# Performance work log

Measured on AMD Instinct MI355X. Metric: run time of the kernel, lower is better.

The kernel has to match this reference:

```python
import jax, jax.numpy as jnp
import numpy as np

# Dims
B, S, D = 4, 4096, 1024
H, NB, A = 4, 4096, 4          # hashes, buckets, associativity
DK, DV, DT = 64, 128, 32        # key dim, value (mem) dim, vsa tag dim
BITS = 12                       # log2(NB)
TEMP = 1.0
VSA_W = 1.0
TANH_SCALE = 1.0
ETA = 0.1
WRITE_THR = 0.5
MATCH_THR = 0.0
NOV_THR = 0.0
EPS = 1e-6


def _l2n(x):
    return x / (jnp.linalg.norm(x, axis=-1, keepdims=True) + EPS)


def setup_inputs() -> dict:
    key = jax.random.key(0)
    ks = jax.random.split(key, 13)
    sc = 0.02
    return {
        "u": jax.random.normal(ks[0], (B, S, D), jnp.float32),
        "memK": jax.random.normal(ks[1], (H, NB, A, DK), jnp.float32),
        "memV": jax.random.normal(ks[2], (H, NB, A, DV), jnp.float32),
        "memT": jnp.tanh(jax.random.normal(ks[3], (H, NB, A, DT), jnp.float32)),
        "Wq": jax.random.normal(ks[4], (DK, D), jnp.float32) * sc,
        "Wwk": jax.random.normal(ks[5], (DK, D), jnp.float32) * sc,
        "Wv": jax.random.normal(ks[6], (DV, D), jnp.float32) * sc,
        "Wo": jax.random.normal(ks[7], (D, DV), jnp.float32) * sc,
        "Wg": jax.random.normal(ks[8], (1, D), jnp.float32) * sc,
        "bg": jnp.zeros((1,), jnp.float32),
        "Wvsa": jax.random.normal(ks[9], (DK, DT), jnp.float32) * sc,
        "R": jax.random.normal(ks[10], (H, DK, BITS), jnp.float32),
    }


def reference(u, memK, memV, memT, Wq, Wwk, Wv, Wo, Wg, bg, Wvsa, R):
    N = B * S
    uf = u.reshape(N, D)

    # ---- routing: sign-bit LSH over query key -> bucket index per hash ----
    qkey = uf @ Wq.T                                     # [N, DK]
    bits = (jnp.einsum("nd,hdk->nhk", qkey, R) > 0).astype(jnp.int32)
    pw = (2 ** jnp.arange(BITS, dtype=jnp.int32))
    idx = (bits * pw).sum(-1)                            # [N, H] bucket ids
    hh = jnp.arange(H)[None, :]                          # [1, H]

    # ---- associative gather read ----
    Kg = memK[hh, idx]                                   # [N, H, A, DK]
    Vg = memV[hh, idx]                                   # [N, H, A, DV]
    Tg = memT[hh, idx]                                   # [N, H, A, DT]
    qtag = jnp.tanh(TANH_SCALE * (qkey @ Wvsa))          # [N, DT]
    sc = (jnp.einsum("nd,nhad->nha", qkey, Kg) / np.sqrt(DK)
          + VSA_W * jnp.einsum("nt,nhat->nha", qtag, Tg) / np.sqrt(DT))
    w = jax.nn.softmax(sc.reshape(N, H * A) / TEMP, axis=-1)
    read = jnp.einsum("nk,nkd->nd", w, Vg.reshape(N, H * A, DV))
    y = (read @ Wo.T).reshape(B, S, D)

    # ---- gated scatter write with EMA + novelty ----
    wkey = uf @ Wwk.T                                    # [N, DK]
    wval = uf @ Wv.T                                     # [N, DV]
    gate = jax.nn.sigmoid(uf @ Wg.T + bg)                # [N, 1]
    wmask = (gate > WRITE_THR).astype(u.dtype)           # [N, 1]
    wtag = jnp.tanh(TANH_SCALE * (wkey @ Wvsa))          # [N, DT]

    sim = jnp.einsum("nd,nhad->nha", _l2n(wkey), _l2n(Kg))   # [N,H,A]
    astar = jnp.argmax(sim, axis=-1)                         # [N,H]
    bsim = jnp.max(sim, axis=-1)                             # [N,H]
    take = lambda G: jnp.take_along_axis(G, astar[:, :, None, None], axis=2)[:, :, 0]
    Kbest, Vbest, Tbest = take(Kg), take(Vg), take(Tg)       # [N,H,·]

    tagsim = jnp.einsum("nt,nhat->nha", _l2n(wtag), _l2n(Tg))
    novelty = 1.0 - jnp.max(tagsim, axis=-1)                 # [N,H]

    eff = (ETA * gate * wmask
           * (bsim >= MATCH_THR).astype(u.dtype)
           * (novelty >= NOV_THR).astype(u.dtype))           # [N,H]

    dK = eff[..., None] * (wkey[:, None, :] - Kbest)
    dV = eff[..., None] * (wval[:, None, :] - Vbest)
    dT = eff[..., None] * (wtag[:, None, :] - Tbest)
    Knew = memK.at[hh, idx, astar].add(dK)
    Vnew = memV.at[hh, idx, astar].add(dV)
    Tnew = memT.at[hh, idx, astar].add(dT)
    return y, Knew, Vnew, Tnew
```

## Files before the change

kernel.cpp:

```cpp
#include <hip/hip_runtime.h>
#include <hip/hip_bf16.h>
#include <math.h>

#define NTOK    16384
#define DMODEL  1024
#define HN      4
#define NBUCKET 4096
#define ASSOC   4
#define DKEY    64
#define DVAL    128
#define DTAG    32
#define NBITS   12
#define EPSV    1e-6f

typedef __bf16 bf16x8 __attribute__((ext_vector_type(8)));
typedef float  f32x4  __attribute__((ext_vector_type(4)));
typedef float  f32x2  __attribute__((ext_vector_type(2)));

__device__ __forceinline__ unsigned short f2bf_raw(float f) {
    __hip_bfloat16 h = __float2bfloat16(f);
    return *(unsigned short*)&h;
}

__global__ __launch_bounds__(256) void gemm_mfma(const float* __restrict__ A,
                                                 const float* __restrict__ B,
                                                 float* __restrict__ C,
                                                 int M, int N, int K) {
    __shared__ __align__(16) unsigned short As[4][128][8];
    __shared__ __align__(16) unsigned short Bs[4][128][8];
    const int t    = threadIdx.x;
    const int lane = t & 63;
    const int w    = t >> 6;
    const int wm   = (w & 1) * 64;
    const int wn   = (w >> 1) * 64;
    const int bm   = blockIdx.x * 128;
    const int bn   = blockIdx.y * 128;

    const int srow = t & 127;
    const int skg  = t >> 7;
    const float* Ap = A + (size_t)(bm + srow) * K;
    const float* Bp = B + (size_t)(bn + srow) * K;

    const int fr = lane & 15;
    const int kq = lane >> 4;

    f32x4 acc[4][4] = {};

    for (int k0 = 0; k0 < K; k0 += 32) {
        #pragma unroll
        for (int ii = 0; ii < 2; ++ii) {
            const int kg = skg + ii * 2;
            const float4 a0 = *(const float4*)(Ap + k0 + kg * 8);
            const float4 a1 = *(const float4*)(Ap + k0 + kg * 8 + 4);
            const float4 b0 = *(const float4*)(Bp + k0 + kg * 8);
            const float4 b1 = *(const float4*)(Bp + k0 + kg * 8 + 4);
            unsigned short* da = &As[kg][srow][0];
            da[0] = f2bf_raw(a0.x); da[1] = f2bf_raw(a0.y);
            da[2] = f2bf_raw(a0.z); da[3] = f2bf_raw(a0.w);
            da[4] = f2bf_raw(a1.x); da[5] = f2bf_raw(a1.y);
            da[6] = f2bf_raw(a1.z); da[7] = f2bf_raw(a1.w);
            unsigned short* db = &Bs[kg][srow][0];
            db[0] = f2bf_raw(b0.x); db[1] = f2bf_raw(b0.y);
            db[2] = f2bf_raw(b0.z); db[3] = f2bf_raw(b0.w);
            db[4] = f2bf_raw(b1.x); db[5] = f2bf_raw(b1.y);
            db[6] = f2bf_raw(b1.z); db[7] = f2bf_raw(b1.w);
        }
        __syncthreads();
        bf16x8 af[4], bfv[4];
        #pragma unroll
        for (int i = 0; i < 4; ++i) af[i]  = *(const bf16x8*)&As[kq][wm + i * 16 + fr][0];
        #pragma unroll
        for (int j = 0; j < 4; ++j) bfv[j] = *(const bf16x8*)&Bs[kq][wn + j * 16 + fr][0];
        #pragma unroll
        for (int i = 0; i < 4; ++i)
            #pragma unroll
            for (int j = 0; j < 4; ++j)
                acc[i][j] = __builtin_amdgcn_mfma_f32_16x16x32_bf16(af[i], bfv[j], acc[i][j], 0, 0, 0);
        __syncthreads();
    }
    #pragma unroll
    for (int i = 0; i < 4; ++i)
        #pragma unroll
        for (int j = 0; j < 4; ++j)
            #pragma unroll
            for (int r = 0; r < 4; ++r)
                C[(size_t)(bm + wm + i * 16 + kq * 4 + r) * N + (bn + wn + j * 16 + fr)] = acc[i][j][r];
}

__global__ __launch_bounds__(256) void gemm_bf16_n64_splitk(const float* __restrict__ A,
                                                            const float* __restrict__ B,
                                                            float* __restrict__ Cpart,
                                                            int M, int K, int K_half) {
    __shared__ __align__(16) unsigned short As[4][128][8];
    __shared__ __align__(16) unsigned short Bs[4][64][8];
    const int t    = threadIdx.x;
    const int lane = t & 63;
    const int w    = t >> 6;
    const int bm   = blockIdx.x * 128;
    const int bn   = blockIdx.y * 64;
    const int kz   = blockIdx.z;

    const int srow = t & 127;
    const int skg  = t >> 7;
    const float* Ap = A + (size_t)(bm + srow) * K;
    const float* Bp = B + (size_t)(bn + (t & 63)) * K;
    const int bkg   = t >> 6;

    const int fr = lane & 15;
    const int kq = lane >> 4;

    f32x4 acc[2][4] = {};

    const int kbeg = kz * K_half, kend = kbeg + K_half;
    for (int k0 = kbeg; k0 < kend; k0 += 32) {
        #pragma unroll
        for (int ii = 0; ii < 2; ++ii) {
            const int kg = skg + ii * 2;
            const float4 a0 = *(const float4*)(Ap + k0 + kg * 8);
            const float4 a1 = *(const float4*)(Ap + k0 + kg * 8 + 4);
            unsigned short* da = &As[kg][srow][0];
            da[0] = f2bf_raw(a0.x); da[1] = f2bf_raw(a0.y);
            da[2] = f2bf_raw(a0.z); da[3] = f2bf_raw(a0.w);
            da[4] = f2bf_raw(a1.x); da[5] = f2bf_raw(a1.y);
            da[6] = f2bf_raw(a1.z); da[7] = f2bf_raw(a1.w);
        }
        {
            const float4 b0 = *(const float4*)(Bp + k0 + bkg * 8);
            const float4 b1 = *(const float4*)(Bp + k0 + bkg * 8 + 4);
            unsigned short* db = &Bs[bkg][t & 63][0];
            db[0] = f2bf_raw(b0.x); db[1] = f2bf_raw(b0.y);
            db[2] = f2bf_raw(b0.z); db[3] = f2bf_raw(b0.w);
            db[4] = f2bf_raw(b1.x); db[5] = f2bf_raw(b1.y);
            db[6] = f2bf_raw(b1.z); db[7] = f2bf_raw(b1.w);
        }
        __syncthreads();
        bf16x8 af[2], bfv[4];
        #pragma unroll
        for (int i = 0; i < 2; ++i) af[i]  = *(const bf16x8*)&As[kq][w * 32 + i * 16 + fr][0];
        #pragma unroll
        for (int j = 0; j < 4; ++j) bfv[j] = *(const bf16x8*)&Bs[kq][j * 16 + fr][0];
        #pragma unroll
        for (int i = 0; i < 2; ++i)
            #pragma unroll
            for (int j = 0; j < 4; ++j)
                acc[i][j] = __builtin_amdgcn_mfma_f32_16x16x32_bf16(af[i], bfv[j], acc[i][j], 0, 0, 0);
        __syncthreads();
    }
    float* Cp = Cpart + (size_t)kz * M * 128;
    #pragma unroll
    for (int i = 0; i < 2; ++i)
        #pragma unroll
        for (int j = 0; j < 4; ++j)
            #pragma unroll
            for (int r = 0; r < 4; ++r)
                Cp[(size_t)(bm + w * 32 + i * 16 + kq * 4 + r) * 128 + (bn + j * 16 + fr)] = acc[i][j][r];
}

__global__ __launch_bounds__(256) void gemm_f32_splitk(const float* __restrict__ A,
                                                       const float* __restrict__ B,
                                                       float* __restrict__ Cpart,
                                                       int M, int K, int K_quarter) {
    __shared__ __align__(16) float As[2][16][68];
    __shared__ __align__(16) float Bs[2][16][140];
    const int t  = threadIdx.x;
    const int bm = blockIdx.x * 64;
    const int kz = blockIdx.z;
    const int tx = t & 15;
    const int ty = t >> 4;

    const int arow = t >> 2, ac = (t & 3) * 4;
    const int brow = t >> 1, bc = (t & 1) * 8;
    const int bperm = brow + ((brow >> 5) << 2);
    const int goff  = tx * 8 + ((tx >> 2) << 2);

    const float* Apt = A + (size_t)(bm + arow) * K + ac;
    const float* Bpt = B + (size_t)brow * K + bc;

    const int kbeg = kz * K_quarter;
    const int NSTEP = 16;

    f32x2 acc2[4][4] = {};

    float4 av = *(const float4*)(Apt + kbeg);
    float4 b0 = *(const float4*)(Bpt + kbeg);
    float4 b1 = *(const float4*)(Bpt + kbeg + 4);
    As[0][ac + 0][arow] = av.x; As[0][ac + 1][arow] = av.y;
    As[0][ac + 2][arow] = av.z; As[0][ac + 3][arow] = av.w;
    Bs[0][bc + 0][bperm] = b0.x; Bs[0][bc + 1][bperm] = b0.y;
    Bs[0][bc + 2][bperm] = b0.z; Bs[0][bc + 3][bperm] = b0.w;
    Bs[0][bc + 4][bperm] = b1.x; Bs[0][bc + 5][bperm] = b1.y;
    Bs[0][bc + 6][bperm] = b1.z; Bs[0][bc + 7][bperm] = b1.w;
    __syncthreads();

    for (int s = 0; s < NSTEP; ++s) {
        const int cur = s & 1;
        if (s + 1 < NSTEP) {
            const int k0 = kbeg + (s + 1) * 16;
            av = *(const float4*)(Apt + k0);
            b0 = *(const float4*)(Bpt + k0);
            b1 = *(const float4*)(Bpt + k0 + 4);
        }
        #pragma unroll
        for (int kk = 0; kk < 16; ++kk) {
            const float4 a4 = *(const float4*)&As[cur][kk][ty * 4];
            const float4 v0 = *(const float4*)&Bs[cur][kk][goff];
            const float4 v1 = *(const float4*)&Bs[cur][kk][goff + 4];
            const float aa[4] = {a4.x, a4.y, a4.z, a4.w};
            const f32x2 bb[4] = {{v0.x, v0.y}, {v0.z, v0.w}, {v1.x, v1.y}, {v1.z, v1.w}};
            #pragma unroll
            for (int i = 0; i < 4; ++i) {
                const f32x2 as2 = {aa[i], aa[i]};
                #pragma unroll
                for (int j = 0; j < 4; ++j)
                    acc2[i][j] = __builtin_elementwise_fma(as2, bb[j], acc2[i][j]);
            }
        }
        if (s + 1 < NSTEP) {
            const int nb = cur ^ 1;
            As[nb][ac + 0][arow] = av.x; As[nb][ac + 1][arow] = av.y;
            As[nb][ac + 2][arow] = av.z; As[nb][ac + 3][arow] = av.w;
            Bs[nb][bc + 0][bperm] = b0.x; Bs[nb][bc + 1][bperm] = b0.y;
            Bs[nb][bc + 2][bperm] = b0.z; Bs[nb][bc + 3][bperm] = b0.w;
            Bs[nb][bc + 4][bperm] = b1.x; Bs[nb][bc + 5][bperm] = b1.y;
            Bs[nb][bc + 6][bperm] = b1.z; Bs[nb][bc + 7][bperm] = b1.w;
        }
        __syncthreads();
    }

    float* Cp = Cpart + (size_t)kz * M * 128;
    #pragma unroll
    for (int i = 0; i < 4; ++i) {
        float4 o0, o1;
        o0.x = acc2[i][0].x; o0.y = acc2[i][0].y; o0.z = acc2[i][1].x; o0.w = acc2[i][1].y;
        o1.x = acc2[i][2].x; o1.y = acc2[i][2].y; o1.z = acc2[i][3].x; o1.w = acc2[i][3].y;
        float* dst = &Cp[(size_t)(bm + ty * 4 + i) * 128 + tx * 8];
        *(float4*)dst       = o0;
        *(float4*)(dst + 4) = o1;
    }
}

__global__ __launch_bounds__(256) void reduce2_kernel(const float* __restrict__ p0,
                                                      const float* __restrict__ p1,
                                                      float* __restrict__ out, int n4) {
    const int i = (blockIdx.x * 256 + threadIdx.x);
    if (i < n4) {
        const float4 a = ((const float4*)p0)[i];
        const float4 b = ((const float4*)p1)[i];
        float4 r; r.x = a.x + b.x; r.y = a.y + b.y; r.z = a.z + b.z; r.w = a.w + b.w;
        ((float4*)out)[i] = r;
    }
}

__global__ __launch_bounds__(256) void reduce4_kernel(const float* __restrict__ p,
                                                      float* __restrict__ out,
                                                      int n4, int stride4) {
    const int i = (blockIdx.x * 256 + threadIdx.x);
    if (i < n4) {
        const float4 a = ((const float4*)p)[i];
        const float4 b = ((const float4*)p)[i + stride4];
        const float4 c = ((const float4*)p)[i + 2 * stride4];
        const float4 d = ((const float4*)p)[i + 3 * stride4];
        float4 r;
        r.x = (a.x + b.x) + (c.x + d.x);
        r.y = (a.y + b.y) + (c.y + d.y);
        r.z = (a.z + b.z) + (c.z + d.z);
        r.w = (a.w + b.w) + (c.w + d.w);
        ((float4*)out)[i] = r;
    }
}

__global__ __launch_bounds__(256) void gate_kernel(const float* __restrict__ u,
                                                   const float* __restrict__ Wg,
                                                   const float* __restrict__ bg,
                                                   float* __restrict__ gateg) {
    const int wv = threadIdx.x >> 6, lane = threadIdx.x & 63;
    const int n = blockIdx.x * 4 + wv;
    const float* up = u + (size_t)n * DMODEL;
    float acc = 0.f;
    #pragma unroll
    for (int j = 0; j < 16; ++j)
        acc += up[lane + 64 * j] * Wg[lane + 64 * j];
    #pragma unroll
    for (int off = 1; off < 64; off <<= 1) acc += __shfl_xor(acc, off);
    if (lane == 0) gateg[n] = 1.f / (1.f + expf(-(acc + bg[0])));
}

__global__ __launch_bounds__(256) void route_kernel(
    const float* __restrict__ memK, const float* __restrict__ memV,
    const float* __restrict__ memT, const float* __restrict__ R,
    const float* __restrict__ Wvsa,
    const float* __restrict__ qw, const float* __restrict__ wvalg,
    const float* __restrict__ gateg,
    float* __restrict__ accK, float* __restrict__ accV, float* __restrict__ accT,
    float* __restrict__ readw) {
    __shared__ float sQK[4][64], sWK[4][64], sQT[4][32], sWT[4][32];
    __shared__ float sSc[4][16], sSim[4][16], sTsim[4][16], sW[4][16];
    __shared__ int   sIdx[4][4], sAst[4][4];
    __shared__ float sEff[4][4];

    const int wv = threadIdx.x >> 6;
    const int lane = threadIdx.x & 63;
    const int n = blockIdx.x * 4 + wv;

    const float qk = qw[(size_t)n * 128 + lane];
    const float wk = qw[(size_t)n * 128 + 64 + lane];
    sQK[wv][lane] = qk;
    sWK[wv][lane] = wk;
    float wk2 = wk * wk;
    #pragma unroll
    for (int off = 1; off < 64; off <<= 1) wk2 += __shfl_xor(wk2, off);
    const float wknorm = sqrtf(wk2) + EPSV;
    __syncthreads();

    {
        const int tg = lane & 31;
        const float* keyp = (lane < 32) ? sQK[wv] : sWK[wv];
        float tacc = 0.f;
        for (int d = 0; d < 64; ++d) tacc += keyp[d] * Wvsa[d * DTAG + tg];
        const float tagv = tanhf(tacc);
        if (lane < 32) sQT[wv][tg] = tagv; else sWT[wv][tg] = tagv;
        float wt2 = (lane >= 32) ? tagv * tagv : 0.f;
        #pragma unroll
        for (int off = 1; off < 64; off <<= 1) wt2 += __shfl_xor(wt2, off);
        const float wtnorm = sqrtf(wt2) + EPSV;

        bool bit = false;
        if (lane < 48) {
            const int h = lane / 12, k = lane % 12;
            float bacc = 0.f;
            for (int d = 0; d < 64; ++d)
                bacc += sQK[wv][d] * R[(size_t)(h * DKEY + d) * NBITS + k];
            bit = bacc > 0.f;
        }
        const unsigned long long mask = __ballot(bit);
        if (lane < 4) sIdx[wv][lane] = (int)((mask >> (12 * lane)) & 0xFFFull);
        __syncthreads();

        const int slot = lane >> 2, sub = lane & 3;
        const int sh = slot >> 2, sa = slot & 3;
        const int rowS = (sh * NBUCKET + sIdx[wv][sh]) * ASSOC + sa;
        const float* Kp = memK + (size_t)rowS * DKEY;
        const float* Tp = memT + (size_t)rowS * DTAG;
        float d_qk = 0, d_wk = 0, d_kk = 0, d_qt = 0, d_wt = 0, d_tt = 0;
        for (int j = 0; j < 16; ++j) {
            const int d = sub * 16 + j;
            const float kv = Kp[d];
            d_qk += sQK[wv][d] * kv;
            d_wk += sWK[wv][d] * kv;
            d_kk += kv * kv;
        }
        for (int j = 0; j < 8; ++j) {
            const int d = sub * 8 + j;
            const float tv = Tp[d];
            d_qt += sQT[wv][d] * tv;
            d_wt += sWT[wv][d] * tv;
            d_tt += tv * tv;
        }
        #pragma unroll
        for (int off = 1; off <= 2; off <<= 1) {
            d_qk += __shfl_xor(d_qk, off);
            d_wk += __shfl_xor(d_wk, off);
            d_kk += __shfl_xor(d_kk, off);
            d_qt += __shfl_xor(d_qt, off);
            d_wt += __shfl_xor(d_wt, off);
            d_tt += __shfl_xor(d_tt, off);
        }
        if (sub == 0) {
            sSc[wv][slot]   = d_qk * 0.125f + d_qt * 0.17677669529663687f;
            sSim[wv][slot]  = d_wk / (wknorm * (sqrtf(d_kk) + EPSV));
            sTsim[wv][slot] = d_wt / (wtnorm * (sqrtf(d_tt) + EPSV));
        }
    }
    __syncthreads();

    if (lane < 16) {
        const float sc = sSc[wv][lane];
        float m = sc;
        #pragma unroll
        for (int off = 1; off < 16; off <<= 1) m = fmaxf(m, __shfl_xor(m, off, 16));
        const float e = expf(sc - m);
        float ssum = e;
        #pragma unroll
        for (int off = 1; off < 16; off <<= 1) ssum += __shfl_xor(ssum, off, 16);
        sW[wv][lane] = e / ssum;
    }
    const float gate = gateg[n];
    if (lane < 4) {
        float bs = -1e30f; int as = 0; float mt = -1e30f;
        #pragma unroll
        for (int aa = 0; aa < 4; ++aa) {
            const float sv = sSim[wv][lane * 4 + aa];
            if (sv > bs) { bs = sv; as = aa; }
            mt = fmaxf(mt, sTsim[wv][lane * 4 + aa]);
        }
        const float novelty = 1.f - mt;
        float e = 0.1f * gate;
        if (!(gate > 0.5f) || !(bs >= 0.f) || !(novelty >= 0.f)) e = 0.f;
        sEff[wv][lane] = e;
        sAst[wv][lane] = as;
    }
    __syncthreads();

    float r0 = 0.f, r1 = 0.f;
    #pragma unroll
    for (int s2 = 0; s2 < 16; ++s2) {
        const int hh = s2 >> 2, aa = s2 & 3;
        const int rw = (hh * NBUCKET + sIdx[wv][hh]) * ASSOC + aa;
        const float wgt = sW[wv][s2];
        const float* Vp = memV + (size_t)rw * DVAL;
        r0 += wgt * Vp[lane];
        r1 += wgt * Vp[64 + lane];
    }
    readw[(size_t)n * DVAL + lane]      = r0;
    readw[(size_t)n * DVAL + 64 + lane] = r1;

    const float wv0 = wvalg[(size_t)n * DVAL + lane];
    const float wv1 = wvalg[(size_t)n * DVAL + 64 + lane];
    for (int hh = 0; hh < 4; ++hh) {
        const float e = sEff[wv][hh];
        if (e == 0.f) continue;
        const int rw = (hh * NBUCKET + sIdx[wv][hh]) * ASSOC + sAst[wv][hh];
        atomicAdd(&accK[(size_t)rw * DKEY + lane],
                  e * (sWK[wv][lane] - memK[(size_t)rw * DKEY + lane]));
        atomicAdd(&accV[(size_t)rw * DVAL + lane],
                  e * (wv0 - memV[(size_t)rw * DVAL + lane]));
        atomicAdd(&accV[(size_t)rw * DVAL + 64 + lane],
                  e * (wv1 - memV[(size_t)rw * DVAL + 64 + lane]));
        if (lane < 32)
            atomicAdd(&accT[(size_t)rw * DTAG + lane],
                      e * (sWT[wv][lane] - memT[(size_t)rw * DTAG + lane]));
    }
}

extern "C" void kernel_launch(void* const* d_in, const int* in_sizes, int n_in,
                              void* d_out, int out_size, void* d_ws, size_t ws_size,
                              hipStream_t stream) {
    const float* u    = (const float*)d_in[0];
    const float* memK = (const float*)d_in[1];
    const float* memV = (const float*)d_in[2];
    const float* memT = (const float*)d_in[3];
    const float* Wq   = (const float*)d_in[4];
    const float* Wwk  = (const float*)d_in[5];
    const float* Wv   = (const float*)d_in[6];
    const float* Wo   = (const float*)d_in[7];
    const float* Wg   = (const float*)d_in[8];
    const float* bg   = (const float*)d_in[9];
    const float* Wvsa = (const float*)d_in[10];
    const float* R    = (const float*)d_in[11];

    const int nK = HN * NBUCKET * ASSOC * DKEY;
    const int nV = HN * NBUCKET * ASSOC * DVAL;
    const int nT = HN * NBUCKET * ASSOC * DTAG;

    float* y_out = (float*)d_out;
    float* K_out = y_out + (size_t)NTOK * DMODEL;
    float* V_out = K_out + nK;
    float* T_out = V_out + nV;

    float* qw    = (float*)d_ws;
    float* wvalg = qw    + (size_t)NTOK * 128;
    float* readw = wvalg + (size_t)NTOK * 128;
    float* gateg = readw + (size_t)NTOK * 128;
    float* qwW   = gateg + NTOK;

    float* part  = y_out;
    float* part2 = y_out + (size_t)4 * NTOK * 128;

    hipMemcpyAsync(qwW,          Wq,  (size_t)DKEY * DMODEL * 4, hipMemcpyDeviceToDevice, stream);
    hipMemcpyAsync(qwW + 65536,  Wwk, (size_t)DKEY * DMODEL * 4, hipMemcpyDeviceToDevice, stream);
    hipMemcpyAsync(K_out, memK, (size_t)nK * 4, hipMemcpyDeviceToDevice, stream);
    hipMemcpyAsync(V_out, memV, (size_t)nV * 4, hipMemcpyDeviceToDevice, stream);
    hipMemcpyAsync(T_out, memT, (size_t)nT * 4, hipMemcpyDeviceToDevice, stream);

    gemm_f32_splitk<<<dim3(NTOK / 64, 1, 4), 256, 0, stream>>>(u, qwW, part, NTOK, DMODEL, DMODEL / 4);
    reduce4_kernel<<<(NTOK * 128 / 4 + 255) / 256, 256, 0, stream>>>(part, qw, NTOK * 128 / 4, NTOK * 128 / 4);
    gemm_bf16_n64_splitk<<<dim3(NTOK / 128, 2, 2), 256, 0, stream>>>(u, Wv, part2, NTOK, DMODEL, DMODEL / 2);
    reduce2_kernel<<<(NTOK * 128 / 4 + 255) / 256, 256, 0, stream>>>(part2, part2 + (size_t)NTOK * 128, wvalg, NTOK * 128 / 4);
    gate_kernel<<<NTOK / 4, 256, 0, stream>>>(u, Wg, bg, gateg);

    route_kernel<<<NTOK / 4, 256, 0, stream>>>(memK, memV, memT, R, Wvsa,
                                               qw, wvalg, gateg,
                                               K_out, V_out, T_out, readw);

    gemm_mfma<<<dim3(NTOK / 128, DMODEL / 128), 256, 0, stream>>>(readw, Wo, y_out, NTOK, DMODEL, DVAL);
}
```

Baseline: 420.4 us.

## Fuse gate projection into fp32 key GEMM and retile both input projections

The fp32 query/write-key GEMM now reads Wq and Wwk directly instead of first copying them into a concatenated workspace. It uses 128-row tiles with an 8-way K split and also accumulates the gate dot product from the staged u tile, which removes the separate gate kernel and its extra pass over u. The bf16 value GEMM becomes a single 128x128 tile per block with a 4-way K split, so u is read fewer times. Partial gate sums are reduced and passed through the sigmoid inside the routing kernel. The costs are more partial-sum traffic (8 partials to reduce), higher register use from the larger per-thread tiles, and reordered memcpys.

```diff
diff --git a/kernel.cpp b/kernel.cpp
--- a/kernel.cpp
+++ b/kernel.cpp
@@ -87,167 +87,177 @@
                 C[(size_t)(bm + wm + i * 16 + kq * 4 + r) * N + (bn + wn + j * 16 + fr)] = acc[i][j][r];
 }
 
-__global__ __launch_bounds__(256) void gemm_bf16_n64_splitk(const float* __restrict__ A,
-                                                            const float* __restrict__ B,
-                                                            float* __restrict__ Cpart,
-                                                            int M, int K, int K_half) {
+__global__ __launch_bounds__(256) void gemm_wval_splitk(const float* __restrict__ A,
+                                                        const float* __restrict__ B,
+                                                        float* __restrict__ Cpart) {
     __shared__ __align__(16) unsigned short As[4][128][8];
-    __shared__ __align__(16) unsigned short Bs[4][64][8];
+    __shared__ __align__(16) unsigned short Bs[4][128][8];
     const int t    = threadIdx.x;
     const int lane = t & 63;
     const int w    = t >> 6;
+    const int wm   = (w & 1) * 64;
+    const int wn   = (w >> 1) * 64;
     const int bm   = blockIdx.x * 128;
-    const int bn   = blockIdx.y * 64;
-    const int kz   = blockIdx.z;
+    const int kz   = blockIdx.y;
+    const int kbeg = kz * 256;
 
     const int srow = t & 127;
     const int skg  = t >> 7;
-    const float* Ap = A + (size_t)(bm + srow) * K;
-    const float* Bp = B + (size_t)(bn + (t & 63)) * K;
-    const int bkg   = t >> 6;
+    const float* Ap = A + (size_t)(bm + srow) * DMODEL;
+    const float* Bp = B + (size_t)srow * DMODEL;
 
     const int fr = lane & 15;
     const int kq = lane >> 4;
 
-    f32x4 acc[2][4] = {};
-
-    const int kbeg = kz * K_half, kend = kbeg + K_half;
-    for (int k0 = kbeg; k0 < kend; k0 += 32) {
+    f32x4 acc[4][4] = {};
+
+    for (int k0 = kbeg; k0 < kbeg + 256; k0 += 32) {
         #pragma unroll
         for (int ii = 0; ii < 2; ++ii) {
             const int kg = skg + ii * 2;
             const float4 a0 = *(const float4*)(Ap + k0 + kg * 8);
             const float4 a1 = *(const float4*)(Ap + k0 + kg * 8 + 4);
+            const float4 b0 = *(const float4*)(Bp + k0 + kg * 8);
+            const float4 b1 = *(const float4*)(Bp + k0 + kg * 8 + 4);
             unsigned short* da = &As[kg][srow][0];
             da[0] = f2bf_raw(a0.x); da[1] = f2bf_raw(a0.y);
             da[2] = f2bf_raw(a0.z); da[3] = f2bf_raw(a0.w);
             da[4] = f2bf_raw(a1.x); da[5] = f2bf_raw(a1.y);
             da[6] = f2bf_raw(a1.z); da[7] = f2bf_raw(a1.w);
-        }
-        {
-            const float4 b0 = *(const float4*)(Bp + k0 + bkg * 8);
-            const float4 b1 = *(const float4*)(Bp + k0 + bkg * 8 + 4);
-            unsigned short* db = &Bs[bkg][t & 63][0];
+            unsigned short* db = &Bs[kg][srow][0];
             db[0] = f2bf_raw(b0.x); db[1] = f2bf_raw(b0.y);
             db[2] = f2bf_raw(b0.z); db[3] = f2bf_raw(b0.w);
             db[4] = f2bf_raw(b1.x); db[5] = f2bf_raw(b1.y);
             db[6] = f2bf_raw(b1.z); db[7] = f2bf_raw(b1.w);
         }
         __syncthreads();
-        bf16x8 af[2], bfv[4];
-        #pragma unroll
-        for (int i = 0; i < 2; ++i) af[i]  = *(const bf16x8*)&As[kq][w * 32 + i * 16 + fr][0];
-        #pragma unroll
-        for (int j = 0; j < 4; ++j) bfv[j] = *(const bf16x8*)&Bs[kq][j * 16 + fr][0];
-        #pragma unroll
-        for (int i = 0; i < 2; ++i)
+        bf16x8 af[4], bfv[4];
+        #pragma unroll
+        for (int i = 0; i < 4; ++i) af[i]  = *(const bf16x8*)&As[kq][wm + i * 16 + fr][0];
+        #pragma unroll
+        for (int j = 0; j < 4; ++j) bfv[j] = *(const bf16x8*)&Bs[kq][wn + j * 16 + fr][0];
+        #pragma unroll
+        for (int i = 0; i < 4; ++i)
             #pragma unroll
             for (int j = 0; j < 4; ++j)
                 acc[i][j] = __builtin_amdgcn_mfma_f32_16x16x32_bf16(af[i], bfv[j], acc[i][j], 0, 0, 0);
         __syncthreads();
     }
-    float* Cp = Cpart + (size_t)kz * M * 128;
+    float* Cp = Cpart + (size_t)kz * NTOK * 128;
     #pragma unroll
-    for (int i = 0; i < 2; ++i)
+    for (int i = 0; i < 4; ++i)
         #pragma unroll
         for (int j = 0; j < 4; ++j)
             #pragma unroll
             for (int r = 0; r < 4; ++r)
-                Cp[(size_t)(bm + w * 32 + i * 16 + kq * 4 + r) * 128 + (bn + j * 16 + fr)] = acc[i][j][r];
-}
-
-__global__ __launch_bounds__(256) void gemm_f32_splitk(const float* __restrict__ A,
-                                                       const float* __restrict__ B,
-                                                       float* __restrict__ Cpart,
-                                                       int M, int K, int K_quarter) {
-    __shared__ __align__(16) float As[2][16][68];
+                Cp[(size_t)(bm + wm + i * 16 + kq * 4 + r) * 128 + (wn + j * 16 + fr)] = acc[i][j][r];
+}
+
+__global__ __launch_bounds__(256) void gemm_f32_128(const float* __restrict__ A,
+                                                    const float* __restrict__ Wq,
+                                                    const float* __restrict__ Wwk,
+                                                    const float* __restrict__ Wg,
+                                                    float* __restrict__ Cpart,
+                                                    float* __restrict__ gatep) {
+    __shared__ __align__(16) float As[2][16][136];
     __shared__ __align__(16) float Bs[2][16][140];
-    const int t  = threadIdx.x;
-    const int bm = blockIdx.x * 64;
-    const int kz = blockIdx.z;
-    const int tx = t & 15;
-    const int ty = t >> 4;
-
-    const int arow = t >> 2, ac = (t & 3) * 4;
-    const int brow = t >> 1, bc = (t & 1) * 8;
-    const int bperm = brow + ((brow >> 5) << 2);
-    const int goff  = tx * 8 + ((tx >> 2) << 2);
-
-    const float* Apt = A + (size_t)(bm + arow) * K + ac;
-    const float* Bpt = B + (size_t)brow * K + bc;
-
-    const int kbeg = kz * K_quarter;
-    const int NSTEP = 16;
-
-    f32x2 acc2[4][4] = {};
-
-    float4 av = *(const float4*)(Apt + kbeg);
-    float4 b0 = *(const float4*)(Bpt + kbeg);
-    float4 b1 = *(const float4*)(Bpt + kbeg + 4);
-    As[0][ac + 0][arow] = av.x; As[0][ac + 1][arow] = av.y;
-    As[0][ac + 2][arow] = av.z; As[0][ac + 3][arow] = av.w;
-    Bs[0][bc + 0][bperm] = b0.x; Bs[0][bc + 1][bperm] = b0.y;
-    Bs[0][bc + 2][bperm] = b0.z; Bs[0][bc + 3][bperm] = b0.w;
-    Bs[0][bc + 4][bperm] = b1.x; Bs[0][bc + 5][bperm] = b1.y;
-    Bs[0][bc + 6][bperm] = b1.z; Bs[0][bc + 7][bperm] = b1.w;
+    __shared__ float sWg[128];
+    const int t    = threadIdx.x;
+    const int bm   = blockIdx.x * 128;
+    const int kz   = blockIdx.z;
+    const int kbeg = kz * 128;
+    const int NSTEP = 8;
+
+    const int tx   = t & 15;
+    const int ty   = t >> 4;
+    const int goff = tx * 8 + ((tx >> 2) << 2);
+
+    const int arow = t >> 1;
+    const int ac8  = (t & 1) * 8;
+    const int bphys = arow + ((arow >> 5) << 2);
+
+    const float* Apt = A + (size_t)(bm + arow) * DMODEL + kbeg + ac8;
+    const float* Bpt = (arow < 64 ? Wq + (size_t)arow * DMODEL
+                                  : Wwk + (size_t)(arow - 64) * DMODEL) + kbeg + ac8;
+
+    if (t < 32) *(float4*)&sWg[t * 4] = *(const float4*)(Wg + kbeg + t * 4);
+
+    f32x2 acc2[8][4] = {};
+    float gacc = 0.f;
+
+    float4 av0 = *(const float4*)(Apt);
+    float4 av1 = *(const float4*)(Apt + 4);
+    float4 bv0 = *(const float4*)(Bpt);
+    float4 bv1 = *(const float4*)(Bpt + 4);
+    As[0][ac8 + 0][arow] = av0.x; As[0][ac8 + 1][arow] = av0.y;
+    As[0][ac8 + 2][arow] = av0.z; As[0][ac8 + 3][arow] = av0.w;
+    As[0][ac8 + 4][arow] = av1.x; As[0][ac8 + 5][arow] = av1.y;
+    As[0][ac8 + 6][arow] = av1.z; As[0][ac8 + 7][arow] = av1.w;
+    Bs[0][ac8 + 0][bphys] = bv0.x; Bs[0][ac8 + 1][bphys] = bv0.y;
+    Bs[0][ac8 + 2][bphys] = bv0.z; Bs[0][ac8 + 3][bphys] = bv0.w;
+    Bs[0][ac8 + 4][bphys] = bv1.x; Bs[0][ac8 + 5][bphys] = bv1.y;
+    Bs[0][ac8 + 6][bphys] = bv1.z; Bs[0][ac8 + 7][bphys] = bv1.w;
     __syncthreads();
 
     for (int s = 0; s < NSTEP; ++s) {
         const int cur = s & 1;
         if (s + 1 < NSTEP) {
-            const int k0 = kbeg + (s + 1) * 16;
-            av = *(const float4*)(Apt + k0);
-            b0 = *(const float4*)(Bpt + k0);
-            b1 = *(const float4*)(Bpt + k0 + 4);
+            av0 = *(const float4*)(Apt + (s + 1) * 16);
+            av1 = *(const float4*)(Apt + (s + 1) * 16 + 4);
+            bv0 = *(const float4*)(Bpt + (s + 1) * 16);
+            bv1 = *(const float4*)(Bpt + (s + 1) * 16 + 4);
         }
         #pragma unroll
         for (int kk = 0; kk < 16; ++kk) {
-            const float4 a4 = *(const float4*)&As[cur][kk][ty * 4];
-            const float4 v0 = *(const float4*)&Bs[cur][kk][goff];
-            const float4 v1 = *(const float4*)&Bs[cur][kk][goff + 4];
-            const float aa[4] = {a4.x, a4.y, a4.z, a4.w};
-            const f32x2 bb[4] = {{v0.x, v0.y}, {v0.z, v0.w}, {v1.x, v1.y}, {v1.z, v1.w}};
+            const float4 a0 = *(const float4*)&As[cur][kk][ty * 8];
+            const float4 a1 = *(const float4*)&As[cur][kk][ty * 8 + 4];
+            const float4 b0 = *(const float4*)&Bs[cur][kk][goff];
+            const float4 b1 = *(const float4*)&Bs[cur][kk][goff + 4];
+            const float ar[8]  = {a0.x, a0.y, a0.z, a0.w, a1.x, a1.y, a1.z, a1.w};
+            const f32x2 br[4]  = {{b0.x, b0.y}, {b0.z, b0.w}, {b1.x, b1.y}, {b1.z, b1.w}};
             #pragma unroll
-            for (int i = 0; i < 4; ++i) {
-                const f32x2 as2 = {aa[i], aa[i]};
+            for (int i = 0; i < 8; ++i) {
+                const f32x2 ai = {ar[i], ar[i]};
                 #pragma unroll
                 for (int j = 0; j < 4; ++j)
-                    acc2[i][j] = __builtin_elementwise_fma(as2, bb[j], acc2[i][j]);
+                    acc2[i][j] = __builtin_elementwise_fma(ai, br[j], acc2[i][j]);
             }
+        }
+        {
+            float ga = 0.f;
+            #pragma unroll
+            for (int kk = 0; kk < 8; ++kk)
+                ga += As[cur][ac8 + kk][arow] * sWg[s * 16 + ac8 + kk];
+            gacc += ga;
         }
         if (s + 1 < NSTEP) {
             const int nb = cur ^ 1;
-            As[nb][ac + 0][arow] = av.x; As[nb][ac + 1][arow] = av.y;
-            As[nb][ac + 2][arow] = av.z; As[nb][ac + 3][arow] = av.w;
-            Bs[nb][bc + 0][bperm] = b0.x; Bs[nb][bc + 1][bperm] = b0.y;
-            Bs[nb][bc + 2][bperm] = b0.z; Bs[nb][bc + 3][bperm] = b0.w;
-            Bs[nb][bc + 4][bperm] = b1.x; Bs[nb][bc + 5][bperm] = b1.y;
-            Bs[nb][bc + 6][bperm] = b1.z; Bs[nb][bc + 7][bperm] = b1.w;
+            As[nb][ac8 + 0][arow] = av0.x; As[nb][ac8 + 1][arow] = av0.y;
+            As[nb][ac8 + 2][arow] = av0.z; As[nb][ac8 + 3][arow] = av0.w;
+            As[nb][ac8 + 4][arow] = av1.x; As[nb][ac8 + 5][arow] = av1.y;
+            As[nb][ac8 + 6][arow] = av1.z; As[nb][ac8 + 7][arow] = av1.w;
+            Bs[nb][ac8 + 0][bphys] = bv0.x; Bs[nb][ac8 + 1][bphys] = bv0.y;
+            Bs[nb][ac8 + 2][bphys] = bv0.z; Bs[nb][ac8 + 3][bphys] = bv0.w;
+            Bs[nb][ac8 + 4][bphys] = bv1.x; Bs[nb][ac8 + 5][bphys] = bv1.y;
+            Bs[nb][ac8 + 6][bphys] = bv1.z; Bs[nb][ac8 + 7][bphys] = bv1.w;
         }
         __syncthreads();
     }
 
-    float* Cp = Cpart + (size_t)kz * M * 128;
+    {
+        const float gtot = gacc + __shfl_xor(gacc, 1);
+        if ((t & 1) == 0) gatep[(size_t)kz * NTOK + bm + arow] = gtot;
+    }
+
+    float* Cp = Cpart + (size_t)kz * NTOK * 128;
     #pragma unroll
-    for (int i = 0; i < 4; ++i) {
+    for (int i = 0; i < 8; ++i) {
         float4 o0, o1;
         o0.x = acc2[i][0].x; o0.y = acc2[i][0].y; o0.z = acc2[i][1].x; o0.w = acc2[i][1].y;
         o1.x = acc2[i][2].x; o1.y = acc2[i][2].y; o1.z = acc2[i][3].x; o1.w = acc2[i][3].y;
-        float* dst = &Cp[(size_t)(bm + ty * 4 + i) * 128 + tx * 8];
+        float* dst = Cp + (size_t)(bm + ty * 8 + i) * 128 + tx * 8;
         *(float4*)dst       = o0;
         *(float4*)(dst + 4) = o1;
-    }
-}
-
-__global__ __launch_bounds__(256) void reduce2_kernel(const float* __restrict__ p0,
-                                                      const float* __restrict__ p1,
-                                                      float* __restrict__ out, int n4) {
-    const int i = (blockIdx.x * 256 + threadIdx.x);
-    if (i < n4) {
-        const float4 a = ((const float4*)p0)[i];
-        const float4 b = ((const float4*)p1)[i];
-        float4 r; r.x = a.x + b.x; r.y = a.y + b.y; r.z = a.z + b.z; r.w = a.w + b.w;
-        ((float4*)out)[i] = r;
     }
 }
 
@@ -269,20 +279,26 @@
     }
 }
 
-__global__ __launch_bounds__(256) void gate_kernel(const float* __restrict__ u,
-                                                   const float* __restrict__ Wg,
-                                                   const float* __restrict__ bg,
-                                                   float* __restrict__ gateg) {
-    const int wv = threadIdx.x >> 6, lane = threadIdx.x & 63;
-    const int n = blockIdx.x * 4 + wv;
-    const float* up = u + (size_t)n * DMODEL;
-    float acc = 0.f;
-    #pragma unroll
-    for (int j = 0; j < 16; ++j)
-        acc += up[lane + 64 * j] * Wg[lane + 64 * j];
-    #pragma unroll
-    for (int off = 1; off < 64; off <<= 1) acc += __shfl_xor(acc, off);
-    if (lane == 0) gateg[n] = 1.f / (1.f + expf(-(acc + bg[0])));
+__global__ __launch_bounds__(256) void reduce8_kernel(const float* __restrict__ p,
+                                                      float* __restrict__ out,
+                                                      int n4, int stride4) {
+    const int i = (blockIdx.x * 256 + threadIdx.x);
+    if (i < n4) {
+        float4 r;
+        const float4 a0 = ((const float4*)p)[i];
+        const float4 a1 = ((const float4*)p)[i + stride4];
+        const float4 a2 = ((const float4*)p)[i + 2 * stride4];
+        const float4 a3 = ((const float4*)p)[i + 3 * stride4];
+        const float4 a4 = ((const float4*)p)[i + 4 * stride4];
+        const float4 a5 = ((const float4*)p)[i + 5 * stride4];
+        const float4 a6 = ((const float4*)p)[i + 6 * stride4];
+        const float4 a7 = ((const float4*)p)[i + 7 * stride4];
+        r.x = ((a0.x + a1.x) + (a2.x + a3.x)) + ((a4.x + a5.x) + (a6.x + a7.x));
+        r.y = ((a0.y + a1.y) + (a2.y + a3.y)) + ((a4.y + a5.y) + (a6.y + a7.y));
+        r.z = ((a0.z + a1.z) + (a2.z + a3.z)) + ((a4.z + a5.z) + (a6.z + a7.z));
+        r.w = ((a0.w + a1.w) + (a2.w + a3.w)) + ((a4.w + a5.w) + (a6.w + a7.w));
+        ((float4*)out)[i] = r;
+    }
 }
 
 __global__ __launch_bounds__(256) void route_kernel(
@@ -290,7 +306,7 @@
     const float* __restrict__ memT, const float* __restrict__ R,
     const float* __restrict__ Wvsa,
     const float* __restrict__ qw, const float* __restrict__ wvalg,
-    const float* __restrict__ gateg,
+    const float* __restrict__ gatep, const float* __restrict__ bg,
     float* __restrict__ accK, float* __restrict__ accV, float* __restrict__ accT,
     float* __restrict__ readw) {
     __shared__ float sQK[4][64], sWK[4][64], sQT[4][32], sWT[4][32];
@@ -384,7 +400,10 @@
         for (int off = 1; off < 16; off <<= 1) ssum += __shfl_xor(ssum, off, 16);
         sW[wv][lane] = e / ssum;
     }
-    const float gate = gateg[n];
+    float gl = bg[0];
+    #pragma unroll
+    for (int z = 0; z < 8; ++z) gl += gatep[(size_t)z * NTOK + n];
+    const float gate = 1.f / (1.f + expf(-gl));
     if (lane < 4) {
         float bs = -1e30f; int as = 0; float mt = -1e30f;
         #pragma unroll
@@ -460,26 +479,22 @@
     float* qw    = (float*)d_ws;
     float* wvalg = qw    + (size_t)NTOK * 128;
     float* readw = wvalg + (size_t)NTOK * 128;
-    float* gateg = readw + (size_t)NTOK * 128;
-    float* qwW   = gateg + NTOK;
-
-    float* part  = y_out;
-    float* part2 = y_out + (size_t)4 * NTOK * 128;
-
-    hipMemcpyAsync(qwW,          Wq,  (size_t)DKEY * DMODEL * 4, hipMemcpyDeviceToDevice, stream);
-    hipMemcpyAsync(qwW + 65536,  Wwk, (size_t)DKEY * DMODEL * 4, hipMemcpyDeviceToDevice, stream);
+    float* gatep = readw + (size_t)NTOK * 128;
+
+    float* part = y_out;
+
+    gemm_f32_128<<<dim3(NTOK / 128, 1, 8), 256, 0, stream>>>(u, Wq, Wwk, Wg, part, gatep);
+    reduce8_kernel<<<(NTOK * 128 / 4 + 255) / 256, 256, 0, stream>>>(part, qw, NTOK * 128 / 4, NTOK * 128 / 4);
+
+    gemm_wval_splitk<<<dim3(NTOK / 128, 4), 256, 0, stream>>>(u, Wv, part);
+    reduce4_kernel<<<(NTOK * 128 / 4 + 255) / 256, 256, 0, stream>>>(part, wvalg, NTOK * 128 / 4, NTOK * 128 / 4);
+
     hipMemcpyAsync(K_out, memK, (size_t)nK * 4, hipMemcpyDeviceToDevice, stream);
     hipMemcpyAsync(V_out, memV, (size_t)nV * 4, hipMemcpyDeviceToDevice, stream);
     hipMemcpyAsync(T_out, memT, (size_t)nT * 4, hipMemcpyDeviceToDevice, stream);
 
-    gemm_f32_splitk<<<dim3(NTOK / 64, 1, 4), 256, 0, stream>>>(u, qwW, part, NTOK, DMODEL, DMODEL / 4);
-    reduce4_kernel<<<(NTOK * 128 / 4 + 255) / 256, 256, 0, stream>>>(part, qw, NTOK * 128 / 4, NTOK * 128 / 4);
-    gemm_bf16_n64_splitk<<<dim3(NTOK / 128, 2, 2), 256, 0, stream>>>(u, Wv, part2, NTOK, DMODEL, DMODEL / 2);
-    reduce2_kernel<<<(NTOK * 128 / 4 + 255) / 256, 256, 0, stream>>>(part2, part2 + (size_t)NTOK * 128, wvalg, NTOK * 128 / 4);
-    gate_kernel<<<NTOK / 4, 256, 0, stream>>>(u, Wg, bg, gateg);
-
     route_kernel<<<NTOK / 4, 256, 0, stream>>>(memK, memV, memT, R, Wvsa,
-                                               qw, wvalg, gateg,
+                                               qw, wvalg, gatep, bg,
                                                K_out, V_out, T_out, readw);
 
     gemm_mfma<<<dim3(NTOK / 128, DMODEL / 128), 256, 0, stream>>>(readw, Wo, y_out, NTOK, DMODEL, DVAL);
```

Result: slower. 447.3 us (+6.4%).

## Fuse split-K reductions and gate into route kernel, widen Wv GEMM tile

Applied to the files above, without the earlier changes.

Removes the separate reduce4, reduce2 and gate kernels. The route kernel now sums the four split-K partials for qkey/wkey and wval itself and computes the sigmoid gate inline from u. The Wv GEMM now covers all 128 output columns per block with a 4-way K split instead of 2x2 N/K blocks, so each u tile is read once. This cuts launches and intermediate round-trips, at the cost of extra partial reads and a 4 KB u row read inside the latency-bound route kernel.

```diff
diff --git a/kernel.cpp b/kernel.cpp
--- a/kernel.cpp
+++ b/kernel.cpp
@@ -87,73 +87,70 @@
                 C[(size_t)(bm + wm + i * 16 + kq * 4 + r) * N + (bn + wn + j * 16 + fr)] = acc[i][j][r];
 }
 
-__global__ __launch_bounds__(256) void gemm_bf16_n64_splitk(const float* __restrict__ A,
-                                                            const float* __restrict__ B,
-                                                            float* __restrict__ Cpart,
-                                                            int M, int K, int K_half) {
+__global__ __launch_bounds__(256) void gemm_wval_splitk(const float* __restrict__ A,
+                                                        const float* __restrict__ B,
+                                                        float* __restrict__ Cpart) {
     __shared__ __align__(16) unsigned short As[4][128][8];
-    __shared__ __align__(16) unsigned short Bs[4][64][8];
+    __shared__ __align__(16) unsigned short Bs[4][128][8];
     const int t    = threadIdx.x;
     const int lane = t & 63;
     const int w    = t >> 6;
+    const int wm   = (w & 1) * 64;
+    const int wn   = (w >> 1) * 64;
     const int bm   = blockIdx.x * 128;
-    const int bn   = blockIdx.y * 64;
-    const int kz   = blockIdx.z;
+    const int kz   = blockIdx.y;
+    const int kbeg = kz * 256;
 
     const int srow = t & 127;
     const int skg  = t >> 7;
-    const float* Ap = A + (size_t)(bm + srow) * K;
-    const float* Bp = B + (size_t)(bn + (t & 63)) * K;
-    const int bkg   = t >> 6;
+    const float* Ap = A + (size_t)(bm + srow) * DMODEL;
+    const float* Bp = B + (size_t)srow * DMODEL;
 
     const int fr = lane & 15;
     const int kq = lane >> 4;
 
-    f32x4 acc[2][4] = {};
-
-    const int kbeg = kz * K_half, kend = kbeg + K_half;
-    for (int k0 = kbeg; k0 < kend; k0 += 32) {
+    f32x4 acc[4][4] = {};
+
+    for (int k0 = kbeg; k0 < kbeg + 256; k0 += 32) {
         #pragma unroll
         for (int ii = 0; ii < 2; ++ii) {
             const int kg = skg + ii * 2;
             const float4 a0 = *(const float4*)(Ap + k0 + kg * 8);
             const float4 a1 = *(const float4*)(Ap + k0 + kg * 8 + 4);
+            const float4 b0 = *(const float4*)(Bp + k0 + kg * 8);
+            const float4 b1 = *(const float4*)(Bp + k0 + kg * 8 + 4);
             unsigned short* da = &As[kg][srow][0];
             da[0] = f2bf_raw(a0.x); da[1] = f2bf_raw(a0.y);
             da[2] = f2bf_raw(a0.z); da[3] = f2bf_raw(a0.w);
             da[4] = f2bf_raw(a1.x); da[5] = f2bf_raw(a1.y);
             da[6] = f2bf_raw(a1.z); da[7] = f2bf_raw(a1.w);
-        }
-        {
-            const float4 b0 = *(const float4*)(Bp + k0 + bkg * 8);
-            const float4 b1 = *(const float4*)(Bp + k0 + bkg * 8 + 4);
-            unsigned short* db = &Bs[bkg][t & 63][0];
+            unsigned short* db = &Bs[kg][srow][0];
             db[0] = f2bf_raw(b0.x); db[1] = f2bf_raw(b0.y);
             db[2] = f2bf_raw(b0.z); db[3] = f2bf_raw(b0.w);
             db[4] = f2bf_raw(b1.x); db[5] = f2bf_raw(b1.y);
             db[6] = f2bf_raw(b1.z); db[7] = f2bf_raw(b1.w);
         }
         __syncthreads();
-        bf16x8 af[2], bfv[4];
-        #pragma unroll
-        for (int i = 0; i < 2; ++i) af[i]  = *(const bf16x8*)&As[kq][w * 32 + i * 16 + fr][0];
-        #pragma unroll
-        for (int j = 0; j < 4; ++j) bfv[j] = *(const bf16x8*)&Bs[kq][j * 16 + fr][0];
-        #pragma unroll
-        for (int i = 0; i < 2; ++i)
+        bf16x8 af[4], bfv[4];
+        #pragma unroll
+        for (int i = 0; i < 4; ++i) af[i]  = *(const bf16x8*)&As[kq][wm + i * 16 + fr][0];
+        #pragma unroll
+        for (int j = 0; j < 4; ++j) bfv[j] = *(const bf16x8*)&Bs[kq][wn + j * 16 + fr][0];
+        #pragma unroll
+        for (int i = 0; i < 4; ++i)
             #pragma unroll
             for (int j = 0; j < 4; ++j)
                 acc[i][j] = __builtin_amdgcn_mfma_f32_16x16x32_bf16(af[i], bfv[j], acc[i][j], 0, 0, 0);
         __syncthreads();
     }
-    float* Cp = Cpart + (size_t)kz * M * 128;
+    float* Cp = Cpart + (size_t)kz * NTOK * 128;
     #pragma unroll
-    for (int i = 0; i < 2; ++i)
+    for (int i = 0; i < 4; ++i)
         #pragma unroll
         for (int j = 0; j < 4; ++j)
             #pragma unroll
             for (int r = 0; r < 4; ++r)
-                Cp[(size_t)(bm + w * 32 + i * 16 + kq * 4 + r) * 128 + (bn + j * 16 + fr)] = acc[i][j][r];
+                Cp[(size_t)(bm + wm + i * 16 + kq * 4 + r) * 128 + (wn + j * 16 + fr)] = acc[i][j][r];
 }
 
 __global__ __launch_bounds__(256) void gemm_f32_splitk(const float* __restrict__ A,
@@ -239,58 +236,13 @@
     }
 }
 
-__global__ __launch_bounds__(256) void reduce2_kernel(const float* __restrict__ p0,
-                                                      const float* __restrict__ p1,
-                                                      float* __restrict__ out, int n4) {
-    const int i = (blockIdx.x * 256 + threadIdx.x);
-    if (i < n4) {
-        const float4 a = ((const float4*)p0)[i];
-        const float4 b = ((const float4*)p1)[i];
-        float4 r; r.x = a.x + b.x; r.y = a.y + b.y; r.z = a.z + b.z; r.w = a.w + b.w;
-        ((float4*)out)[i] = r;
-    }
-}
-
-__global__ __launch_bounds__(256) void reduce4_kernel(const float* __restrict__ p,
-                                                      float* __restrict__ out,
-                                                      int n4, int stride4) {
-    const int i = (blockIdx.x * 256 + threadIdx.x);
-    if (i < n4) {
-        const float4 a = ((const float4*)p)[i];
-        const float4 b = ((const float4*)p)[i + stride4];
-        const float4 c = ((const float4*)p)[i + 2 * stride4];
-        const float4 d = ((const float4*)p)[i + 3 * stride4];
-        float4 r;
-        r.x = (a.x + b.x) + (c.x + d.x);
-        r.y = (a.y + b.y) + (c.y + d.y);
-        r.z = (a.z + b.z) + (c.z + d.z);
-        r.w = (a.w + b.w) + (c.w + d.w);
-        ((float4*)out)[i] = r;
-    }
-}
-
-__global__ __launch_bounds__(256) void gate_kernel(const float* __restrict__ u,
-                                                   const float* __restrict__ Wg,
-                                                   const float* __restrict__ bg,
-                                                   float* __restrict__ gateg) {
-    const int wv = threadIdx.x >> 6, lane = threadIdx.x & 63;
-    const int n = blockIdx.x * 4 + wv;
-    const float* up = u + (size_t)n * DMODEL;
-    float acc = 0.f;
-    #pragma unroll
-    for (int j = 0; j < 16; ++j)
-        acc += up[lane + 64 * j] * Wg[lane + 64 * j];
-    #pragma unroll
-    for (int off = 1; off < 64; off <<= 1) acc += __shfl_xor(acc, off);
-    if (lane == 0) gateg[n] = 1.f / (1.f + expf(-(acc + bg[0])));
-}
-
 __global__ __launch_bounds__(256) void route_kernel(
     const float* __restrict__ memK, const float* __restrict__ memV,
     const float* __restrict__ memT, const float* __restrict__ R,
     const float* __restrict__ Wvsa,
-    const float* __restrict__ qw, const float* __restrict__ wvalg,
-    const float* __restrict__ gateg,
+    const float* __restrict__ partQ, const float* __restrict__ partW,
+    const float* __restrict__ u, const float* __restrict__ Wg,
+    const float* __restrict__ bg,
     float* __restrict__ accK, float* __restrict__ accV, float* __restrict__ accT,
     float* __restrict__ readw) {
     __shared__ float sQK[4][64], sWK[4][64], sQT[4][32], sWT[4][32];
@@ -301,15 +253,30 @@
     const int wv = threadIdx.x >> 6;
     const int lane = threadIdx.x & 63;
     const int n = blockIdx.x * 4 + wv;
-
-    const float qk = qw[(size_t)n * 128 + lane];
-    const float wk = qw[(size_t)n * 128 + 64 + lane];
+    const size_t PZ = (size_t)NTOK * 128;
+
+    const size_t qb = (size_t)n * 128;
+    const float qk = (partQ[qb + lane]          + partQ[PZ + qb + lane])
+                   + (partQ[2 * PZ + qb + lane] + partQ[3 * PZ + qb + lane]);
+    const float wk = (partQ[qb + 64 + lane]          + partQ[PZ + qb + 64 + lane])
+                   + (partQ[2 * PZ + qb + 64 + lane] + partQ[3 * PZ + qb + 64 + lane]);
     sQK[wv][lane] = qk;
     sWK[wv][lane] = wk;
     float wk2 = wk * wk;
     #pragma unroll
     for (int off = 1; off < 64; off <<= 1) wk2 += __shfl_xor(wk2, off);
     const float wknorm = sqrtf(wk2) + EPSV;
+
+    float gacc = 0.f;
+    {
+        const float* up = u + (size_t)n * DMODEL;
+        #pragma unroll
+        for (int j = 0; j < 16; ++j)
+            gacc += up[lane + 64 * j] * Wg[lane + 64 * j];
+        #pragma unroll
+        for (int off = 1; off < 64; off <<= 1) gacc += __shfl_xor(gacc, off);
+    }
+    const float gate = 1.f / (1.f + expf(-(gacc + bg[0])));
     __syncthreads();
 
     {
@@ -384,7 +351,6 @@
         for (int off = 1; off < 16; off <<= 1) ssum += __shfl_xor(ssum, off, 16);
         sW[wv][lane] = e / ssum;
     }
-    const float gate = gateg[n];
     if (lane < 4) {
         float bs = -1e30f; int as = 0; float mt = -1e30f;
         #pragma unroll
@@ -414,8 +380,10 @@
     readw[(size_t)n * DVAL + lane]      = r0;
     readw[(size_t)n * DVAL + 64 + lane] = r1;
 
-    const float wv0 = wvalg[(size_t)n * DVAL + lane];
-    const float wv1 = wvalg[(size_t)n * DVAL + 64 + lane];
+    const float wv0 = (partW[qb + lane]          + partW[PZ + qb + lane])
+                    + (partW[2 * PZ + qb + lane] + partW[3 * PZ + qb + lane]);
+    const float wv1 = (partW[qb + 64 + lane]          + partW[PZ + qb + 64 + lane])
+                    + (partW[2 * PZ + qb + 64 + lane] + partW[3 * PZ + qb + 64 + lane]);
     for (int hh = 0; hh < 4; ++hh) {
         const float e = sEff[wv][hh];
         if (e == 0.f) continue;
@@ -457,29 +425,25 @@
     float* V_out = K_out + nK;
     float* T_out = V_out + nV;
 
-    float* qw    = (float*)d_ws;
-    float* wvalg = qw    + (size_t)NTOK * 128;
-    float* readw = wvalg + (size_t)NTOK * 128;
-    float* gateg = readw + (size_t)NTOK * 128;
-    float* qwW   = gateg + NTOK;
-
-    float* part  = y_out;
-    float* part2 = y_out + (size_t)4 * NTOK * 128;
+    float* readw = (float*)d_ws;
+    float* qwW   = readw + (size_t)NTOK * 128;
+
+    float* partQ = y_out;
+    float* partW = y_out + (size_t)4 * NTOK * 128;
 
     hipMemcpyAsync(qwW,          Wq,  (size_t)DKEY * DMODEL * 4, hipMemcpyDeviceToDevice, stream);
     hipMemcpyAsync(qwW + 65536,  Wwk, (size_t)DKEY * DMODEL * 4, hipMemcpyDeviceToDevice, stream);
+
+    gemm_f32_splitk<<<dim3(NTOK / 64, 1, 4), 256, 0, stream>>>(u, qwW, partQ, NTOK, DMODEL, DMODEL / 4);
+
+    gemm_wval_splitk<<<dim3(NTOK / 128, 4), 256, 0, stream>>>(u, Wv, partW);
+
     hipMemcpyAsync(K_out, memK, (size_t)nK * 4, hipMemcpyDeviceToDevice, stream);
     hipMemcpyAsync(V_out, memV, (size_t)nV * 4, hipMemcpyDeviceToDevice, stream);
     hipMemcpyAsync(T_out, memT, (size_t)nT * 4, hipMemcpyDeviceToDevice, stream);
 
-    gemm_f32_splitk<<<dim3(NTOK / 64, 1, 4), 256, 0, stream>>>(u, qwW, part, NTOK, DMODEL, DMODEL / 4);
-    reduce4_kernel<<<(NTOK * 128 / 4 + 255) / 256, 256, 0, stream>>>(part, qw, NTOK * 128 / 4, NTOK * 128 / 4);
-    gemm_bf16_n64_splitk<<<dim3(NTOK / 128, 2, 2), 256, 0, stream>>>(u, Wv, part2, NTOK, DMODEL, DMODEL / 2);
-    reduce2_kernel<<<(NTOK * 128 / 4 + 255) / 256, 256, 0, stream>>>(part2, part2 + (size_t)NTOK * 128, wvalg, NTOK * 128 / 4);
-    gate_kernel<<<NTOK / 4, 256, 0, stream>>>(u, Wg, bg, gateg);
-
     route_kernel<<<NTOK / 4, 256, 0, stream>>>(memK, memV, memT, R, Wvsa,
-                                               qw, wvalg, gateg,
+                                               partQ, partW, u, Wg, bg,
                                                K_out, V_out, T_out, readw);
 
     gemm_mfma<<<dim3(NTOK / 128, DMODEL / 128), 256, 0, stream>>>(readw, Wo, y_out, NTOK, DMODEL, DVAL);
```

Result: faster. 401.3 us (-4.6%).
